# Optimization experiments

Hardware: AMD Instinct MI355X
Metric: run time of the kernel (lower is better)

## Reference

```python
import jax, jax.numpy as jnp
import numpy as np

NA, NT, E = 8000, 30000, 150000
H, C, HID = 4, 64, 64  # heads, per-head out_channels, hidden_dim
AF, TF = 32, 48


def _gat(x_src, x_dst, src, dst, W, a_src, a_dst, bias, n_dst):
    # PyG GATConv, concat=False, add_self_loops=False, eval (no dropout)
    h_src = (x_src @ W).reshape(-1, H, C)          # [Ns,H,C]
    h_dst = (x_dst @ W).reshape(-1, H, C)          # [Nd,H,C]
    al_s = jnp.sum(h_src * a_src, axis=-1)         # [Ns,H]
    al_d = jnp.sum(h_dst * a_dst, axis=-1)         # [Nd,H]
    e = jax.nn.leaky_relu(al_s[src] + al_d[dst], 0.2)  # [E,H]
    m = jax.ops.segment_max(e, dst, num_segments=n_dst)
    m = jnp.where(jnp.isfinite(m), m, 0.0)
    ex = jnp.exp(e - m[dst])
    den = jax.ops.segment_sum(ex, dst, num_segments=n_dst)
    alpha = ex / (den[dst] + 1e-16)                # per-dst softmax
    out = jax.ops.segment_sum(alpha[:, :, None] * h_src[src], dst, num_segments=n_dst)
    return jnp.mean(out, axis=1) + bias            # mean over heads + bias


def _bn(x, g, b):  # BatchNorm1d, training-mode batch stats, biased var
    mu = jnp.mean(x, axis=0)
    v = jnp.var(x, axis=0)
    return g * (x - mu) * jax.lax.rsqrt(v + 1e-5) + b


def _ln(x, g, b):
    mu = jnp.mean(x, axis=-1, keepdims=True)
    v = jnp.var(x, axis=-1, keepdims=True)
    return g * (x - mu) * jax.lax.rsqrt(v + 1e-5) + b


def setup_inputs() -> dict:
    key = jax.random.key(0)
    ks = jax.random.split(key, 40)
    n = lambda i, shp, s=0.05: jax.random.normal(ks[i], shp, jnp.float32) * s
    ri = lambda i, hi: jax.random.randint(ks[i], (E,), 0, hi, jnp.int32)
    inp = {
        'x_agent': jax.random.normal(ks[0], (NA, AF), jnp.float32),
        'x_track': jax.random.normal(ks[1], (NT, TF), jnp.float32),
        'ei_a2t1_src': ri(2, NA), 'ei_a2t1_dst': ri(3, NT),
        'ei_t2a1_src': ri(4, NT), 'ei_t2a1_dst': ri(5, NA),
        'ei_a2t2_src': ri(6, NA), 'ei_a2t2_dst': ri(7, NT),
        'ei_t2a2_src': ri(8, NT), 'ei_t2a2_dst': ri(9, NA),
        'ae_W': n(10, (AF, HID)), 'ae_b': jnp.zeros((HID,), jnp.float32),
        'te_W': n(11, (TF, HID)), 'te_b': jnp.zeros((HID,), jnp.float32),
        # stacked GATConv params: [layer=3, relation=4, ...]; rel order: a2t1,t2a1,a2t2,t2a2
        'conv_W': n(12, (3, 4, HID, H * C)),
        'conv_asrc': n(13, (3, 4, H, C)),
        'conv_adst': n(14, (3, 4, H, C)),
        'conv_bias': jnp.zeros((3, 4, C), jnp.float32),
        'bn_gamma': jnp.ones((3, 2, HID), jnp.float32),   # [layer, agent/track, HID]
        'bn_beta': jnp.zeros((3, 2, HID), jnp.float32),
        # actor heads: 0=agent_alpha,1=agent_beta,2=track_alpha,3=track_beta
        'actor_W1': n(15, (4, HID, HID // 2)), 'actor_b1': jnp.zeros((4, HID // 2), jnp.float32),
        'actor_g': jnp.ones((4, HID // 2), jnp.float32), 'actor_be': jnp.zeros((4, HID // 2), jnp.float32),
        'actor_W2': n(16, (4, HID // 2, 1)), 'actor_b2': jnp.zeros((4, 1), jnp.float32),
        # critic global value head
        'cW1': n(17, (HID * 6, HID * 2)), 'cb1': jnp.zeros((HID * 2,), jnp.float32),
        'cg1': jnp.ones((HID * 2,), jnp.float32), 'cbe1': jnp.zeros((HID * 2,), jnp.float32),
        'cW2': n(18, (HID * 2, HID)), 'cb2': jnp.zeros((HID,), jnp.float32),
        'cg2': jnp.ones((HID,), jnp.float32), 'cbe2': jnp.zeros((HID,), jnp.float32),
        'cW3': n(19, (HID, HID // 2)), 'cb3': jnp.zeros((HID // 2,), jnp.float32),
        'cW4': n(20, (HID // 2, 1)), 'cb4': jnp.zeros((1,), jnp.float32),
    }
    return inp


def _forward(x_agent, x_track,
             ei_a2t1_src, ei_a2t1_dst, ei_t2a1_src, ei_t2a1_dst,
             ei_a2t2_src, ei_a2t2_dst, ei_t2a2_src, ei_t2a2_dst,
             ae_W, ae_b, te_W, te_b,
             conv_W, conv_asrc, conv_adst, conv_bias,
             bn_gamma, bn_beta,
             actor_W1, actor_b1, actor_g, actor_be, actor_W2, actor_b2,
             cW1, cb1, cg1, cbe1, cW2, cb2, cg2, cbe2, cW3, cb3, cW4, cb4):
    xa = jax.nn.relu(x_agent @ ae_W + ae_b)
    xt = jax.nn.relu(x_track @ te_W + te_b)
    prev_a, prev_t = None, None
    for l in range(3):
        # HeteroConv aggr='mean': track <- mean(rel0, rel2); agent <- mean(rel1, rel3)
        ot = 0.5 * (_gat(xa, xt, ei_a2t1_src, ei_a2t1_dst, conv_W[l, 0], conv_asrc[l, 0], conv_adst[l, 0], conv_bias[l, 0], NT)
                    + _gat(xa, xt, ei_a2t2_src, ei_a2t2_dst, conv_W[l, 2], conv_asrc[l, 2], conv_adst[l, 2], conv_bias[l, 2], NT))
        oa = 0.5 * (_gat(xt, xa, ei_t2a1_src, ei_t2a1_dst, conv_W[l, 1], conv_asrc[l, 1], conv_adst[l, 1], conv_bias[l, 1], NA)
                    + _gat(xt, xa, ei_t2a2_src, ei_t2a2_dst, conv_W[l, 3], conv_asrc[l, 3], conv_adst[l, 3], conv_bias[l, 3], NA))
        oa = _bn(jax.nn.relu(oa), bn_gamma[l, 0], bn_beta[l, 0])
        ot = _bn(jax.nn.relu(ot), bn_gamma[l, 1], bn_beta[l, 1])
        if l > 0:  # residuals after layers 2 and 3
            oa = oa + prev_a
            ot = ot + prev_t
        prev_a, prev_t = oa, ot
        xa, xt = oa, ot

    def head(x, i):
        h = jax.nn.relu(_ln(x @ actor_W1[i] + actor_b1[i], actor_g[i], actor_be[i]))
        return jax.nn.softplus(h @ actor_W2[i] + actor_b2[i]) + 1.0

    aA, aB = head(xa, 0), head(xa, 1)
    tA, tB = head(xt, 2), head(xt, 3)
    aC = aA / (aA + aB)
    tC = tA / (tA + tB)

    # critic global value (torch.std is unbiased, ddof=1)
    g = jnp.concatenate([
        jnp.mean(xa, axis=0), jnp.max(xa, axis=0), jnp.std(xa, axis=0, ddof=1),
        jnp.mean(xt, axis=0), jnp.max(xt, axis=0), jnp.std(xt, axis=0, ddof=1)], axis=0)[None, :]
    h = jax.nn.relu(_ln(g @ cW1 + cb1, cg1, cbe1))
    h = jax.nn.relu(_ln(h @ cW2 + cb2, cg2, cbe2))
    h = jax.nn.relu(h @ cW3 + cb3)
    gv = jnp.squeeze(h @ cW4 + cb4)
    return aA, aB, aC, tA, tB, tC, gv


def reference(x_agent, x_track,
              ei_a2t1_src, ei_a2t1_dst, ei_t2a1_src, ei_t2a1_dst,
              ei_a2t2_src, ei_a2t2_dst, ei_t2a2_src, ei_t2a2_dst,
              ae_W, ae_b, te_W, te_b,
              conv_W, conv_asrc, conv_adst, conv_bias,
              bn_gamma, bn_beta,
              actor_W1, actor_b1, actor_g, actor_be, actor_W2, actor_b2,
              cW1, cb1, cg1, cbe1, cW2, cb2, cg2, cbe2, cW3, cb3, cW4, cb4):
    return _forward(x_agent, x_track,
                    ei_a2t1_src, ei_a2t1_dst, ei_t2a1_src, ei_t2a1_dst,
                    ei_a2t2_src, ei_a2t2_dst, ei_t2a2_src, ei_t2a2_dst,
                    ae_W, ae_b, te_W, te_b,
                    conv_W, conv_asrc, conv_adst, conv_bias,
                    bn_gamma, bn_beta,
                    actor_W1, actor_b1, actor_g, actor_be, actor_W2, actor_b2,
                    cW1, cb1, cg1, cbe1, cW2, cb2, cg2, cbe2, cW3, cb3, cW4, cb4)
```

## Files before the change

kernel.cpp:

```cpp
#include <hip/hip_runtime.h>
#include <math.h>

#define NAg 8000
#define NTr 30000
#define NE  150000

#define XA_OFF 0
#define XT_OFF 512000
#define H0_OFF 2432000
#define H1_OFF 4480000
#define H2_OFF 12160000
#define H3_OFF 14208000
#define BNSTB 8320000
#define ALS0 21888000
#define ALS1 21920000
#define ALS2 22040000
#define ALS3 22072000
#define ALD0 22192000
#define ALD1 22312000
#define ALD2 22344000
#define ALD3 22464000
#define ESRC_I 22496000
#define OAACC 23104000
#define OTACC 23616000
#define BNST 25536000
#define CST  25536256
#define ROWP_I 25536640
#define CURS_I 25656704
#define RELSTRIDE 30016

typedef unsigned short ushortT;

__device__ __forceinline__ float lrelu(float x){ return x >= 0.f ? x : 0.2f*x; }
__device__ __forceinline__ unsigned fmap(float f){ unsigned u=__float_as_uint(f); return (u&0x80000000u)? ~u : (u|0x80000000u); }
__device__ __forceinline__ float funmap(unsigned u){ return (u&0x80000000u)? __uint_as_float(u&0x7FFFFFFFu) : __uint_as_float(~u); }
__device__ __forceinline__ float softplusf(float x){ return fmaxf(x,0.f) + log1pf(expf(-fabsf(x))); }
__device__ __forceinline__ ushortT f2bf(float f){
  unsigned u = __float_as_uint(f);
  unsigned r = u + 0x7FFFu + ((u>>16)&1u);
  return (ushortT)(r>>16);
}
__device__ __forceinline__ float bf2f(ushortT s){ return __uint_as_float(((unsigned)s)<<16); }
__device__ __forceinline__ float wred64(float v){
  #pragma unroll
  for (int o=32;o;o>>=1) v += __shfl_xor(v,o);
  return v;
}
__device__ __forceinline__ float wred32(float v){
  #pragma unroll
  for (int o=16;o;o>>=1) v += __shfl_xor(v,o,32);
  return v;
}
__device__ __forceinline__ int selH(int r){ return r==0?H0_OFF: r==1?H1_OFF: r==2?H2_OFF:H3_OFF; }
__device__ __forceinline__ int selALS(int r){ return r==0?ALS0: r==1?ALS1: r==2?ALS2:ALS3; }
__device__ __forceinline__ int selALD(int r){ return r==0?ALD0: r==1?ALD1: r==2?ALD2:ALD3; }

__global__ __launch_bounds__(256) void k_encoder(const float* xA, const float* xT,
    const float* aeW, const float* aeB, const float* teW, const float* teB, float* ws) {
  int type = blockIdx.y;
  int N = type ? NTr : NAg;
  int t = threadIdx.x, wv = t >> 6, lane = t & 63;
  int n = blockIdx.x*4 + wv;
  int F = type ? 48 : 32;
  const float* X = type ? xT : xA;
  const float* W = type ? teW : aeW;
  const float* B = type ? teB : aeB;
  float* out = ws + (type ? XT_OFF : XA_OFF);
  __shared__ float xs[4][48];
  if (n < N && lane < F) xs[wv][lane] = X[(size_t)n*F + lane];
  __syncthreads();
  if (n >= N) return;
  float acc = B[lane];
  for (int k = 0; k < F; ++k) acc += xs[wv][k] * W[k*64 + lane];
  out[(size_t)n*64 + lane] = fmaxf(acc, 0.f);
}

__global__ __launch_bounds__(256) void k_hist(const int* d0_,const int* d1_,const int* d2_,const int* d3_,
                                              int* wsi) {
  int r = blockIdx.y;
  const int* dp = r==0? d0_ : r==1? d1_ : r==2? d2_ : d3_;
  int e = blockIdx.x*256 + threadIdx.x;
  if (e >= NE) return;
  atomicAdd(&wsi[ROWP_I + r*RELSTRIDE + dp[e]], 1);
}

__global__ __launch_bounds__(256) void k_scan(int* wsi) {
  int r = blockIdx.x;
  int n = ((r & 1) ? NAg : NTr) + 1;
  int* rp = wsi + ROWP_I + r*RELSTRIDE;
  __shared__ int part[256];
  int t = threadIdx.x;
  int chunk = (n + 255) / 256;
  int lo = t*chunk, hi = min(lo + chunk, n);
  int s = 0;
  for (int i = lo; i < hi; ++i) s += rp[i];
  part[t] = s;
  __syncthreads();
  if (t == 0) {
    int run = 0;
    for (int i = 0; i < 256; ++i) { int tm = part[i]; part[i] = run; run += tm; }
  }
  __syncthreads();
  int run = part[t];
  for (int i = lo; i < hi; ++i) { int tm = rp[i]; rp[i] = run; run += tm; }
}

__global__ __launch_bounds__(256) void k_fill(const int* s0,const int* d0_,const int* s1,const int* d1_,
    const int* s2,const int* d2_,const int* s3,const int* d3_, int* wsi) {
  int r = blockIdx.y;
  const int* sp = r==0? s0 : r==1? s1 : r==2? s2 : s3;
  const int* dp = r==0? d0_ : r==1? d1_ : r==2? d2_ : d3_;
  int e = blockIdx.x*256 + threadIdx.x;
  if (e >= NE) return;
  int d = dp[e];
  int pos = wsi[ROWP_I + r*RELSTRIDE + d] + atomicAdd(&wsi[CURS_I + r*RELSTRIDE + d], 1);
  wsi[ESRC_I + r*NE + pos] = sp[e];
}

__global__ __launch_bounds__(256) void k_ald(const float* convW, const float* convAdst,
                                             float* ws, int layer) {
  int r = blockIdx.y;
  int Nd = (r & 1) ? NAg : NTr;
  const float* W  = convW + (size_t)(layer*4 + r)*64*256;
  const float* ad = convAdst + (size_t)(layer*4 + r)*256;
  __shared__ float Wad[64*4];
  int t = threadIdx.x;
  {
    int k = t >> 2, h = t & 3;
    float s = 0.f;
    for (int c = 0; c < 64; ++c) s += W[k*256 + h*64 + c] * ad[h*64 + c];
    Wad[k*4 + h] = s;
  }
  __syncthreads();
  const float* xd = ws + ((r & 1) ? XA_OFF : XT_OFF);
  float* ald = ws + selALD(r);
  int n = blockIdx.x * 64 + (t >> 2);
  if (n >= Nd) return;
  int h = t & 3;
  float s = 0.f;
  for (int k = 0; k < 64; ++k) s += xd[n*64 + k] * Wad[k*4 + h];
  ald[n*4 + h] = s;
}

__global__ __launch_bounds__(256) void k_h_als(const float* convW, const float* convAsrc,
                                               float* ws, int layer) {
  int r = blockIdx.y;
  int Ns = (r & 1) ? NTr : NAg;
  int row0 = blockIdx.x * 16;
  if (row0 >= Ns) return;
  const float* W  = convW + (size_t)(layer*4 + r)*64*256;
  const float* as = convAsrc + (size_t)(layer*4 + r)*256;
  const float* xg = ws + ((r & 1) ? XT_OFF : XA_OFF);
  ushortT* h16 = (ushortT*)(ws + selH(r));
  float* als = ws + selALS(r);
  __shared__ float xs[16][64];
  __shared__ float asl[256];
  int t = threadIdx.x;
  asl[t] = as[t];
  #pragma unroll
  for (int i = 0; i < 4; ++i) {
    int lin = i*256 + t;
    xs[lin>>6][lin&63] = xg[(row0 + (lin>>6))*64 + (lin&63)];
  }
  __syncthreads();
  int c0 = t & 63;
  int tr = t >> 6;
  float acc[4][4];
  #pragma unroll
  for (int i=0;i<4;i++){ acc[i][0]=0;acc[i][1]=0;acc[i][2]=0;acc[i][3]=0; }
  const float* Wc = W + c0;
  for (int k4 = 0; k4 < 16; ++k4) {
    float4 xv[4];
    #pragma unroll
    for (int i = 0; i < 4; ++i) xv[i] = *(const float4*)&xs[tr*4+i][k4*4];
    #pragma unroll
    for (int kk = 0; kk < 4; ++kk) {
      int k = k4*4 + kk;
      float w0 = Wc[k*256], w1 = Wc[k*256+64], w2 = Wc[k*256+128], w3 = Wc[k*256+192];
      #pragma unroll
      for (int i = 0; i < 4; ++i) {
        float x = (kk==0)?xv[i].x:(kk==1)?xv[i].y:(kk==2)?xv[i].z:xv[i].w;
        acc[i][0] += x*w0; acc[i][1] += x*w1; acc[i][2] += x*w2; acc[i][3] += x*w3;
      }
    }
  }
  #pragma unroll
  for (int i = 0; i < 4; ++i) {
    int row = row0 + tr*4 + i;
    ushort4 pk;
    pk.x = f2bf(acc[i][0]); pk.y = f2bf(acc[i][1]);
    pk.z = f2bf(acc[i][2]); pk.w = f2bf(acc[i][3]);
    *(ushort4*)(h16 + (size_t)row*256 + c0*4) = pk;
  }
  #pragma unroll
  for (int i = 0; i < 4; ++i) {
    #pragma unroll
    for (int j = 0; j < 4; ++j) {
      float v = acc[i][j] * asl[j*64 + c0];
      v = wred64(v);
      if (c0 == 0) als[(row0 + tr*4 + i)*4 + j] = v;
    }
  }
}

__global__ __launch_bounds__(256) void k_agg(const float* convBias, float* ws, int layer) {
  int type = blockIdx.y;
  int N = type ? NAg : NTr;
  if (blockIdx.x * 4 >= N) return;
  int t = threadIdx.x, lane = t & 63, hh = lane & 3, base = lane & ~3;
  int node = blockIdx.x*4 + (t >> 6);
  const int* wsi = (const int*)ws;
  float outv = 0.f;
  #pragma unroll
  for (int rr = 0; rr < 2; ++rr) {
    int r = type ? (rr ? 3 : 1) : (rr ? 2 : 0);
    const int* rp = wsi + ROWP_I + r*RELSTRIDE;
    const int* es = wsi + ESRC_I + r*NE;
    const float* als = ws + selALS(r);
    const ushortT* h16 = (const ushortT*)(ws + selH(r));
    float ad = (ws + selALD(r))[node*4 + hh];
    int p = rp[node], p1 = rp[node+1];
    float num0=0.f, num1=0.f, num2=0.f, num3=0.f, den=0.f;
    for (; p + 4 <= p1; p += 4) {
      int sa = es[p], sb = es[p+1], sc = es[p+2], sd4 = es[p+3];
      ushort4 va = *(const ushort4*)(h16 + (size_t)sa*256 + lane*4);
      ushort4 vb = *(const ushort4*)(h16 + (size_t)sb*256 + lane*4);
      ushort4 vc = *(const ushort4*)(h16 + (size_t)sc*256 + lane*4);
      ushort4 vd = *(const ushort4*)(h16 + (size_t)sd4*256 + lane*4);
      float la = als[sa*4+hh], lb = als[sb*4+hh], lc = als[sc*4+hh], ld = als[sd4*4+hh];
      float ea = __expf(lrelu(la + ad));
      float eb = __expf(lrelu(lb + ad));
      float ec = __expf(lrelu(lc + ad));
      float ed = __expf(lrelu(ld + ad));
      den += (ea+eb)+(ec+ed);
      float qa0=__shfl(ea,base), qa1=__shfl(ea,base+1), qa2=__shfl(ea,base+2), qa3=__shfl(ea,base+3);
      float qb0=__shfl(eb,base), qb1=__shfl(eb,base+1), qb2=__shfl(eb,base+2), qb3=__shfl(eb,base+3);
      float qc0=__shfl(ec,base), qc1=__shfl(ec,base+1), qc2=__shfl(ec,base+2), qc3=__shfl(ec,base+3);
      float qd0=__shfl(ed,base), qd1=__shfl(ed,base+1), qd2=__shfl(ed,base+2), qd3=__shfl(ed,base+3);
      num0 += qa0*bf2f(va.x) + qb0*bf2f(vb.x) + qc0*bf2f(vc.x) + qd0*bf2f(vd.x);
      num1 += qa1*bf2f(va.y) + qb1*bf2f(vb.y) + qc1*bf2f(vc.y) + qd1*bf2f(vd.y);
      num2 += qa2*bf2f(va.z) + qb2*bf2f(vb.z) + qc2*bf2f(vc.z) + qd2*bf2f(vd.z);
      num3 += qa3*bf2f(va.w) + qb3*bf2f(vb.w) + qc3*bf2f(vc.w) + qd3*bf2f(vd.w);
    }
    for (; p < p1; ++p) {
      int s = es[p];
      ushort4 va = *(const ushort4*)(h16 + (size_t)s*256 + lane*4);
      float e = __expf(lrelu(als[s*4 + hh] + ad));
      den += e;
      float q0 = __shfl(e, base), q1 = __shfl(e, base+1), q2 = __shfl(e, base+2), q3 = __shfl(e, base+3);
      num0 += q0*bf2f(va.x); num1 += q1*bf2f(va.y); num2 += q2*bf2f(va.z); num3 += q3*bf2f(va.w);
    }
    float rd = 1.f/(den + 1e-16f);
    float r0 = __shfl(rd, base), r1 = __shfl(rd, base+1), r2 = __shfl(rd, base+2), r3 = __shfl(rd, base+3);
    outv += num0*r0 + num1*r1 + num2*r2 + num3*r3;
  }
  int rA = type ? 1 : 0, rB = type ? 3 : 2;
  float bavg = 0.5f*(convBias[(layer*4 + rA)*64 + lane] + convBias[(layer*4 + rB)*64 + lane]);
  float z = fmaxf(outv*0.125f + bavg, 0.f);
  float* acc = ws + (type ? OAACC : OTACC);
  acc[(size_t)node*64 + lane] = z;
  __shared__ float sdm[2][256];
  sdm[0][t] = z; sdm[1][t] = z*z;
  __syncthreads();
  if (t < 64) {
    float s1 = sdm[0][t] + sdm[0][t+64] + sdm[0][t+128] + sdm[0][t+192];
    float s2 = sdm[1][t] + sdm[1][t+64] + sdm[1][t+128] + sdm[1][t+192];
    int bt = type ? 0 : 1;
    int bucket = blockIdx.x & 63;
    atomicAdd(&ws[BNSTB + bucket*256 + bt*128 + t], s1);
    atomicAdd(&ws[BNSTB + bucket*256 + bt*128 + 64 + t], s2);
  }
}

__global__ __launch_bounds__(256) void k_bnred(float* ws) {
  int t = threadIdx.x;
  float s = 0.f;
  #pragma unroll
  for (int b = 0; b < 64; ++b) s += ws[BNSTB + b*256 + t];
  ws[BNST + t] = s;
}

__global__ __launch_bounds__(256) void k_bnnorm(const float* bnG, const float* bnB, float* ws, int layer) {
  int type = blockIdx.y;
  int N = type ? NTr : NAg;
  float* acc = ws + (type ? OTACC : OAACC);
  float* x = ws + (type ? XT_OFF : XA_OFF);
  int i = blockIdx.x*256 + threadIdx.x;
  if (i >= N*64) return;
  int c = i & 63;
  float Nf = (float)N;
  float s1 = ws[BNST + type*128 + c], s2 = ws[BNST + type*128 + 64 + c];
  float mu = s1/Nf, var = s2/Nf - mu*mu;
  float g = bnG[(layer*2 + type)*64 + c], b = bnB[(layer*2 + type)*64 + c];
  float y = g*(acc[i]-mu)*rsqrtf(var + 1e-5f) + b;
  if (layer > 0) y += x[i];
  x[i] = y;
}

__global__ __launch_bounds__(256) void k_actor(const float* aW1, const float* ab1, const float* ag,
    const float* abe, const float* aW2, const float* ab2, const float* ws, float* out) {
  int type = blockIdx.y;
  int N = type ? NTr : NAg;
  int t = threadIdx.x, wv = t >> 6, lane = t & 63;
  int p = lane >> 5, j = lane & 31;
  int n = blockIdx.x*4 + wv;
  const float* xg = ws + (type ? XT_OFF : XA_OFF);
  __shared__ float xsh[4][64];
  {
    int nn = blockIdx.x*4 + (t >> 6);
    if (nn < N) xsh[t >> 6][t & 63] = xg[(size_t)nn*64 + (t & 63)];
  }
  __syncthreads();
  if (n >= N) return;
  int i = (type ? 2 : 0) + p;
  const float* W = aW1 + i*2048 + j;
  float a0 = 0.f, a1 = 0.f, a2 = 0.f, a3 = 0.f;
  #pragma unroll
  for (int k = 0; k < 64; k += 4) {
    a0 += xsh[wv][k]   * W[k*32];
    a1 += xsh[wv][k+1] * W[(k+1)*32];
    a2 += xsh[wv][k+2] * W[(k+2)*32];
    a3 += xsh[wv][k+3] * W[(k+3)*32];
  }
  float tv = ((a0+a1)+(a2+a3)) + ab1[i*32 + j];
  float mu = wred32(tv) * (1.f/32.f);
  float dz = tv - mu;
  float var = wred32(dz*dz) * (1.f/32.f);
  float hn = fmaxf(ag[i*32+j]*dz*rsqrtf(var + 1e-5f) + abe[i*32+j], 0.f);
  float s = wred32(hn * aW2[i*32 + j]) + ab2[i];
  float val = softplusf(s) + 1.f;
  float vA = __shfl(val, 0);
  float vB = __shfl(val, 32);
  if (lane == 0) {
    int offA = type ? 24000 : 0, offB = type ? 54000 : 8000, offC = type ? 84000 : 16000;
    out[offA + n] = vA;
    out[offB + n] = vB;
    out[offC + n] = vA / (vA + vB);
  }
}

__global__ __launch_bounds__(256) void k_criticstats(float* ws) {
  int type = blockIdx.y;
  int N = type ? NTr : NAg;
  const float* x = ws + (type ? XT_OFF : XA_OFF);
  int t = threadIdx.x;
  int c = t & 63;
  float s1 = 0.f, s2 = 0.f, mx = -3.4e38f;
  for (int n = blockIdx.x*4 + (t>>6); n < N; n += gridDim.x*4) {
    float v = x[(size_t)n*64 + c];
    s1 += v; s2 += v*v; mx = fmaxf(mx, v);
  }
  __shared__ float sd[3][256];
  sd[0][t]=s1; sd[1][t]=s2; sd[2][t]=mx;
  __syncthreads();
  if (t < 64) {
    s1 = sd[0][t]+sd[0][t+64]+sd[0][t+128]+sd[0][t+192];
    s2 = sd[1][t]+sd[1][t+64]+sd[1][t+128]+sd[1][t+192];
    mx = fmaxf(fmaxf(sd[2][t],sd[2][t+64]), fmaxf(sd[2][t+128],sd[2][t+192]));
    atomicAdd(&ws[CST + type*192 + c], s1);
    atomicAdd(&ws[CST + type*192 + 64 + c], s2);
    atomicMax((unsigned*)&ws[CST + type*192 + 128 + c], fmap(mx));
  }
}

__device__ __forceinline__ float blocksum128(float v, float* red) {
  int t = threadIdx.x;
  red[t] = v; __syncthreads();
  #pragma unroll
  for (int s = 64; s > 0; s >>= 1) { if (t < s) red[t] += red[t+s]; __syncthreads(); }
  float r = red[0]; __syncthreads();
  return r;
}

__global__ __launch_bounds__(128) void k_critic(const float* cW1,const float* cb1,const float* cg1,const float* cbe1,
    const float* cW2,const float* cb2,const float* cg2,const float* cbe2,
    const float* cW3,const float* cb3,const float* cW4,const float* cb4,
    const float* ws, float* out) {
  __shared__ float g[384];
  __shared__ float h1[128];
  __shared__ float h2s[64];
  __shared__ float red[128];
  int t = threadIdx.x;
  if (t < 64) {
    #pragma unroll
    for (int type = 0; type < 2; ++type) {
      float Nf = type ? 30000.f : 8000.f;
      float s1 = ws[CST + type*192 + t];
      float s2 = ws[CST + type*192 + 64 + t];
      unsigned mu_ = __float_as_uint(ws[CST + type*192 + 128 + t]);
      float mean = s1 / Nf;
      float sd = sqrtf(fmaxf((s2 - Nf*mean*mean) / (Nf - 1.f), 0.f));
      g[type*192 + t] = mean;
      g[type*192 + 64 + t] = funmap(mu_);
      g[type*192 + 128 + t] = sd;
    }
  }
  __syncthreads();
  float v = cb1[t];
  for (int k = 0; k < 384; ++k) v += g[k] * cW1[k*128 + t];
  float mu = blocksum128(v, red) * (1.f/128.f);
  float d = v - mu;
  float var = blocksum128(d*d, red) * (1.f/128.f);
  h1[t] = fmaxf(cg1[t]*d*rsqrtf(var + 1e-5f) + cbe1[t], 0.f);
  __syncthreads();
  float v2 = 0.f;
  if (t < 64) { v2 = cb2[t]; for (int k = 0; k < 128; ++k) v2 += h1[k] * cW2[k*64 + t]; }
  float mu2 = blocksum128(t < 64 ? v2 : 0.f, red) * (1.f/64.f);
  float d2 = v2 - mu2;
  float var2 = blocksum128(t < 64 ? d2*d2 : 0.f, red) * (1.f/64.f);
  if (t < 64) h2s[t] = fmaxf(cg2[t]*d2*rsqrtf(var2 + 1e-5f) + cbe2[t], 0.f);
  __syncthreads();
  float v3 = 0.f;
  if (t < 32) {
    v3 = cb3[t];
    for (int k = 0; k < 64; ++k) v3 += h2s[k] * cW3[k*32 + t];
    v3 = fmaxf(v3, 0.f);
  }
  float s4 = blocksum128(t < 32 ? v3 * cW4[t] : 0.f, red);
  if (t == 0) out[114000] = s4 + cb4[0];
}

extern "C" void kernel_launch(void* const* d_in, const int* in_sizes, int n_in,
                              void* d_out, int out_size, void* d_ws, size_t ws_size,
                              hipStream_t stream) {
  const float* x_agent = (const float*)d_in[0];
  const float* x_track = (const float*)d_in[1];
  const int* s0 = (const int*)d_in[2]; const int* d0_ = (const int*)d_in[3];
  const int* s1 = (const int*)d_in[4]; const int* d1_ = (const int*)d_in[5];
  const int* s2 = (const int*)d_in[6]; const int* d2_ = (const int*)d_in[7];
  const int* s3 = (const int*)d_in[8]; const int* d3_ = (const int*)d_in[9];
  const float* aeW = (const float*)d_in[10]; const float* aeB = (const float*)d_in[11];
  const float* teW = (const float*)d_in[12]; const float* teB = (const float*)d_in[13];
  const float* convW    = (const float*)d_in[14];
  const float* convAsrc = (const float*)d_in[15];
  const float* convAdst = (const float*)d_in[16];
  const float* convBias = (const float*)d_in[17];
  const float* bnG = (const float*)d_in[18]; const float* bnB = (const float*)d_in[19];
  const float* aW1 = (const float*)d_in[20]; const float* ab1 = (const float*)d_in[21];
  const float* ag  = (const float*)d_in[22]; const float* abe = (const float*)d_in[23];
  const float* aW2 = (const float*)d_in[24]; const float* ab2 = (const float*)d_in[25];
  const float* cW1 = (const float*)d_in[26]; const float* cb1 = (const float*)d_in[27];
  const float* cg1 = (const float*)d_in[28]; const float* cbe1 = (const float*)d_in[29];
  const float* cW2 = (const float*)d_in[30]; const float* cb2 = (const float*)d_in[31];
  const float* cg2 = (const float*)d_in[32]; const float* cbe2 = (const float*)d_in[33];
  const float* cW3 = (const float*)d_in[34]; const float* cb3 = (const float*)d_in[35];
  const float* cW4 = (const float*)d_in[36]; const float* cb4 = (const float*)d_in[37];
  float* ws = (float*)d_ws;
  int* wsi = (int*)d_ws;
  float* out = (float*)d_out;

  hipMemsetAsync(wsi + ROWP_I, 0, (size_t)240128 * sizeof(int), stream);
  hipMemsetAsync(ws + CST, 0, (size_t)384 * sizeof(float), stream);

  k_encoder<<<dim3(7500, 2), 256, 0, stream>>>(x_agent, x_track, aeW, aeB, teW, teB, ws);

  k_hist<<<dim3(586, 4), 256, 0, stream>>>(d0_, d1_, d2_, d3_, wsi);
  k_scan<<<dim3(4), 256, 0, stream>>>(wsi);
  k_fill<<<dim3(586, 4), 256, 0, stream>>>(s0,d0_,s1,d1_,s2,d2_,s3,d3_, wsi);

  for (int l = 0; l < 3; ++l) {
    hipMemsetAsync(ws + BNSTB, 0, (size_t)16384 * sizeof(float), stream);
    k_ald<<<dim3(469, 4), 256, 0, stream>>>(convW, convAdst, ws, l);
    k_h_als<<<dim3(1875, 4), 256, 0, stream>>>(convW, convAsrc, ws, l);
    k_agg<<<dim3(7500, 2), 256, 0, stream>>>(convBias, ws, l);
    k_bnred<<<1, 256, 0, stream>>>(ws);
    k_bnnorm<<<dim3(7500, 2), 256, 0, stream>>>(bnG, bnB, ws, l);
  }

  k_criticstats<<<dim3(128, 2), 256, 0, stream>>>(ws);
  k_actor<<<dim3(7500, 2), 256, 0, stream>>>(aW1, ab1, ag, abe, aW2, ab2, ws, out);
  k_critic<<<1, 128, 0, stream>>>(cW1,cb1,cg1,cbe1,cW2,cb2,cg2,cbe2,cW3,cb3,cW4,cb4, ws, out);
}
```

Measured before the change: 677.1 us.

## Compute source attention logits via folded W·a and compact GEMM grid

The source-side attention logits are no longer computed inside the projection GEMM with a wave-wide shuffle reduction. They are now obtained by folding W with a_src into a 64x4 matrix and doing a small matvec, in the same kernel as the destination logits. The projection GEMM drops the reduction epilogue and uses a flat 1D grid that enumerates only the valid tiles of each relation, which avoids launching empty blocks. The logits are now computed from fp32 inputs instead of the accumulators, at the cost of re-reading the source features once more.

```diff
diff --git a/kernel.cpp b/kernel.cpp
--- a/kernel.cpp
+++ b/kernel.cpp
@@ -41,11 +41,6 @@
   return (ushortT)(r>>16);
 }
 __device__ __forceinline__ float bf2f(ushortT s){ return __uint_as_float(((unsigned)s)<<16); }
-__device__ __forceinline__ float wred64(float v){
-  #pragma unroll
-  for (int o=32;o;o>>=1) v += __shfl_xor(v,o);
-  return v;
-}
 __device__ __forceinline__ float wred32(float v){
   #pragma unroll
   for (int o=16;o;o>>=1) v += __shfl_xor(v,o,32);
@@ -117,50 +112,50 @@
   wsi[ESRC_I + r*NE + pos] = sp[e];
 }
 
-__global__ __launch_bounds__(256) void k_ald(const float* convW, const float* convAdst,
-                                             float* ws, int layer) {
-  int r = blockIdx.y;
-  int Nd = (r & 1) ? NAg : NTr;
+__global__ __launch_bounds__(256) void k_alx(const float* convW, const float* convAsrc,
+                                             const float* convAdst, float* ws, int layer) {
+  int y = blockIdx.y;
+  int side = y >> 2;
+  int r = y & 3;
+  int Nn = side ? ((r & 1) ? NTr : NAg) : ((r & 1) ? NAg : NTr);
+  if (blockIdx.x * 64 >= Nn) return;
   const float* W  = convW + (size_t)(layer*4 + r)*64*256;
-  const float* ad = convAdst + (size_t)(layer*4 + r)*256;
-  __shared__ float Wad[64*4];
+  const float* av = (side ? convAsrc : convAdst) + (size_t)(layer*4 + r)*256;
+  __shared__ float Wv[64*4];
   int t = threadIdx.x;
   {
     int k = t >> 2, h = t & 3;
     float s = 0.f;
-    for (int c = 0; c < 64; ++c) s += W[k*256 + h*64 + c] * ad[h*64 + c];
-    Wad[k*4 + h] = s;
-  }
-  __syncthreads();
-  const float* xd = ws + ((r & 1) ? XA_OFF : XT_OFF);
-  float* ald = ws + selALD(r);
+    for (int c = 0; c < 64; ++c) s += W[k*256 + h*64 + c] * av[h*64 + c];
+    Wv[k*4 + h] = s;
+  }
+  __syncthreads();
+  const float* xv = ws + (side ? ((r & 1) ? XT_OFF : XA_OFF) : ((r & 1) ? XA_OFF : XT_OFF));
+  float* outp = ws + (side ? selALS(r) : selALD(r));
   int n = blockIdx.x * 64 + (t >> 2);
-  if (n >= Nd) return;
+  if (n >= Nn) return;
   int h = t & 3;
   float s = 0.f;
-  for (int k = 0; k < 64; ++k) s += xd[n*64 + k] * Wad[k*4 + h];
-  ald[n*4 + h] = s;
-}
-
-__global__ __launch_bounds__(256) void k_h_als(const float* convW, const float* convAsrc,
-                                               float* ws, int layer) {
-  int r = blockIdx.y;
-  int Ns = (r & 1) ? NTr : NAg;
-  int row0 = blockIdx.x * 16;
-  if (row0 >= Ns) return;
+  for (int k = 0; k < 64; ++k) s += xv[(size_t)n*64 + k] * Wv[k*4 + h];
+  outp[n*4 + h] = s;
+}
+
+__global__ __launch_bounds__(256) void k_hgemm(const float* convW, float* ws, int layer) {
+  int tile = blockIdx.x;
+  int r, row0;
+  if (tile < 500)        { r = 0; row0 = tile*16; }
+  else if (tile < 2375)  { r = 1; row0 = (tile-500)*16; }
+  else if (tile < 2875)  { r = 2; row0 = (tile-2375)*16; }
+  else                   { r = 3; row0 = (tile-2875)*16; }
   const float* W  = convW + (size_t)(layer*4 + r)*64*256;
-  const float* as = convAsrc + (size_t)(layer*4 + r)*256;
   const float* xg = ws + ((r & 1) ? XT_OFF : XA_OFF);
   ushortT* h16 = (ushortT*)(ws + selH(r));
-  float* als = ws + selALS(r);
   __shared__ float xs[16][64];
-  __shared__ float asl[256];
-  int t = threadIdx.x;
-  asl[t] = as[t];
+  int t = threadIdx.x;
   #pragma unroll
   for (int i = 0; i < 4; ++i) {
     int lin = i*256 + t;
-    xs[lin>>6][lin&63] = xg[(row0 + (lin>>6))*64 + (lin&63)];
+    xs[lin>>6][lin&63] = xg[((size_t)row0 + (lin>>6))*64 + (lin&63)];
   }
   __syncthreads();
   int c0 = t & 63;
@@ -191,15 +186,6 @@
     pk.x = f2bf(acc[i][0]); pk.y = f2bf(acc[i][1]);
     pk.z = f2bf(acc[i][2]); pk.w = f2bf(acc[i][3]);
     *(ushort4*)(h16 + (size_t)row*256 + c0*4) = pk;
-  }
-  #pragma unroll
-  for (int i = 0; i < 4; ++i) {
-    #pragma unroll
-    for (int j = 0; j < 4; ++j) {
-      float v = acc[i][j] * asl[j*64 + c0];
-      v = wred64(v);
-      if (c0 == 0) als[(row0 + tr*4 + i)*4 + j] = v;
-    }
   }
 }
 
@@ -460,8 +446,8 @@
 
   for (int l = 0; l < 3; ++l) {
     hipMemsetAsync(ws + BNSTB, 0, (size_t)16384 * sizeof(float), stream);
-    k_ald<<<dim3(469, 4), 256, 0, stream>>>(convW, convAdst, ws, l);
-    k_h_als<<<dim3(1875, 4), 256, 0, stream>>>(convW, convAsrc, ws, l);
+    k_alx<<<dim3(469, 8), 256, 0, stream>>>(convW, convAsrc, convAdst, ws, l);
+    k_hgemm<<<dim3(4750), 256, 0, stream>>>(convW, ws, l);
     k_agg<<<dim3(7500, 2), 256, 0, stream>>>(convBias, ws, l);
     k_bnred<<<1, 256, 0, stream>>>(ws);
     k_bnnorm<<<dim3(7500, 2), 256, 0, stream>>>(bnG, bnB, ws, l);
```

Measured after the change: 678.1 us. Within noise of the previous version (+0.1%).
